# Performance work log

Hardware: AMD Instinct MI355X
Metric: run time of the kernel (lower is better)

Reference implementation:

```python
import jax, jax.numpy as jnp
import numpy as np
from jax import lax

J2 = -1.0
J4 = 0.5
KT = 0.5
DT = 0.01
SIGMA = float(np.sqrt(2.0 * KT * DT))  # noise scale per Euler-Maruyama step


def setup_inputs() -> dict:
    key = jax.random.key(0)
    k_x, = jax.random.split(key, 1)
    n_samples, n_dim = 2048, 256
    x0 = jax.random.normal(k_x, (n_samples, n_dim), dtype=jnp.float32)
    b = jnp.zeros((n_dim,), dtype=jnp.float32)  # learned bias parameter
    return {"x0": x0, "b": b, "n_steps": 500}


def reference(x0, b, n_steps):
    # Langevin dynamics: x <- x - grad_V(x)*dt + sqrt(2 kT dt)*N(0,1)
    # grad_V(x) = 2*J2*x + 4*J4*x^3 + b
    keys = jax.random.split(jax.random.key(1), n_steps)

    def step(x, k):
        grad = 2.0 * J2 * x + 4.0 * J4 * x * x * x + b
        noise = jax.random.normal(k, x.shape, x.dtype) * SIGMA
        return x - grad * DT + noise, None

    x, _ = lax.scan(step, x0, keys)
    return x
```

## Files before the change

### kernel.cpp

```cpp
#include <hip/hip_runtime.h>


__device__ __forceinline__ void tf2x32(unsigned k0, unsigned k1,
                                       unsigned c0, unsigned c1,
                                       unsigned& o0, unsigned& o1) {
  const unsigned k2 = k0 ^ k1 ^ 0x1BD11BDAu;
  unsigned x0 = c0 + k0, x1 = c1 + k1;
#define TF1(R) x0 += x1; x1 = ((x1 << (R)) | (x1 >> (32 - (R)))); x1 ^= x0;
  TF1(13) TF1(15) TF1(26) TF1(6)  x0 += k1; x1 += k2 + 1u;
  TF1(17) TF1(29) TF1(16) TF1(24) x0 += k2; x1 += k0 + 2u;
  TF1(13) TF1(15) TF1(26) TF1(6)  x0 += k0; x1 += k1 + 3u;
  TF1(17) TF1(29) TF1(16) TF1(24) x0 += k1; x1 += k2 + 4u;
  TF1(13) TF1(15) TF1(26) TF1(6)  x0 += k2; x1 += k0 + 5u;
#undef TF1
  o0 = x0; o1 = x1;
}

__device__ __forceinline__ void tf_fold2k(const unsigned wa[8],
                                          const unsigned wb[8], unsigned cj,
                                          unsigned& ra, unsigned& rb) {
  unsigned a0 = wa[0], a1 = cj + wa[1];
  unsigned b0 = wb[0], b1 = cj + wb[1];
#define TFR2(R)                                   \
  a0 += a1; b0 += b1;                             \
  a1 = ((a1 << (R)) | (a1 >> (32 - (R)))) ^ a0;   \
  b1 = ((b1 << (R)) | (b1 >> (32 - (R)))) ^ b0;
#define TFINJ2(i0, i1) a0 += wa[i0]; b0 += wb[i0]; a1 += wa[i1]; b1 += wb[i1];
  TFR2(13) TFR2(15) TFR2(26) TFR2(6)  TFINJ2(1, 3)
  TFR2(17) TFR2(29) TFR2(16) TFR2(24) TFINJ2(2, 4)
  TFR2(13) TFR2(15) TFR2(26) TFR2(6)  TFINJ2(0, 5)
  TFR2(17) TFR2(29) TFR2(16) TFR2(24) TFINJ2(1, 6)
  TFR2(13) TFR2(15) TFR2(26) TFR2(6)  TFINJ2(2, 7)
#undef TFR2
#undef TFINJ2
  ra = a0 ^ a1;
  rb = b0 ^ b1;
}

__device__ __forceinline__ void b2n2(unsigned bba, unsigned bbb,
                                     float& na, float& nb) {
  const float fa = __uint_as_float((bba >> 9) | 0x3F800000u) - 1.0f;
  const float fb = __uint_as_float((bbb >> 9) | 0x3F800000u) - 1.0f;
  const float ua = fmaf(fa, 2.0f, -0.99999994f);
  const float ub = fmaf(fb, 2.0f, -0.99999994f);
  const float ma = ua * ua, mb = ub * ub;
  const float la = __log2f(1.0f - ma);
  const float lb = __log2f(1.0f - mb);
  const float wa = la * -0.693147180559945f;
  const float wb = lb * -0.693147180559945f;
  const bool sa = wa < 5.0f, sb = wb < 5.0f;
  const float za = sa ? (wa - 2.5f) : (__builtin_amdgcn_sqrtf(wa) - 3.0f);
  const float zb = sb ? (wb - 2.5f) : (__builtin_amdgcn_sqrtf(wb) - 3.0f);
  float pa =           sa ? 2.81022636e-08f  : -0.000200214257f;
  float pb =           sb ? 2.81022636e-08f  : -0.000200214257f;
  pa = fmaf(pa, za,    sa ? 3.43273939e-07f  :  0.000100950558f);
  pb = fmaf(pb, zb,    sb ? 3.43273939e-07f  :  0.000100950558f);
  pa = fmaf(pa, za,    sa ? -3.5233877e-06f  :  0.00134934322f);
  pb = fmaf(pb, zb,    sb ? -3.5233877e-06f  :  0.00134934322f);
  pa = fmaf(pa, za,    sa ? -4.39150654e-06f : -0.00367342844f);
  pb = fmaf(pb, zb,    sb ? -4.39150654e-06f : -0.00367342844f);
  pa = fmaf(pa, za,    sa ? 0.00021858087f   :  0.00573950773f);
  pb = fmaf(pb, zb,    sb ? 0.00021858087f   :  0.00573950773f);
  pa = fmaf(pa, za,    sa ? -0.00125372503f  : -0.0076224613f);
  pb = fmaf(pb, zb,    sb ? -0.00125372503f  : -0.0076224613f);
  pa = fmaf(pa, za,    sa ? -0.00417768164f  :  0.00943887047f);
  pb = fmaf(pb, zb,    sb ? -0.00417768164f  :  0.00943887047f);
  pa = fmaf(pa, za,    sa ? 0.246640727f     :  1.00167406f);
  pb = fmaf(pb, zb,    sb ? 0.246640727f     :  1.00167406f);
  pa = fmaf(pa, za,    sa ? 1.50140941f      :  2.83297682f);
  pb = fmaf(pb, zb,    sb ? 1.50140941f      :  2.83297682f);
  na = __uint_as_float(0x3FB504F3u) * (pa * ua);
  nb = __uint_as_float(0x3FB504F3u) * (pb * ub);
}

__global__ __launch_bounds__(256, 8) void langevin_tf(
    const float* __restrict__ x0p, const float* __restrict__ bias,
    const int* __restrict__ nsteps_p, float* __restrict__ out,
    int N, int ndim) {
  __shared__ __align__(16) unsigned skeys[512 * 8];
  const int n_steps = __builtin_amdgcn_readfirstlane(nsteps_p[0]);
  const int nfill = n_steps < 512 ? n_steps : 512;
  for (int l = (int)threadIdx.x; l < nfill; l += (int)blockDim.x) {
    unsigned o0, o1;
    tf2x32(0u, 1u, 0u, (unsigned)l, o0, o1);
    const unsigned k2 = o0 ^ o1 ^ 0x1BD11BDAu;
    unsigned* wp = &skeys[8 * l];
    wp[0] = o0;       wp[1] = o1;       wp[2] = k2;       wp[3] = k2 + 1u;
    wp[4] = o0 + 2u;  wp[5] = o1 + 3u;  wp[6] = k2 + 4u;  wp[7] = o0 + 5u;
  }
  __syncthreads();

  const int j = (int)(blockIdx.x * blockDim.x + threadIdx.x);
  if (j >= N) return;
  const unsigned cj = (unsigned)j;
  float x = x0p[j];
  const float b = bias[j % ndim];

  if (n_steps <= 512) {
    const uint4* sk4 = (const uint4*)skeys;
    int t = 0;
#pragma unroll 1
    for (; t + 1 < n_steps; t += 2) {
      const uint4 a_lo = sk4[2 * t + 0], a_hi = sk4[2 * t + 1];
      const uint4 b_lo = sk4[2 * t + 2], b_hi = sk4[2 * t + 3];
      const unsigned wa[8] = {a_lo.x, a_lo.y, a_lo.z, a_lo.w,
                              a_hi.x, a_hi.y, a_hi.z, a_hi.w};
      const unsigned wb[8] = {b_lo.x, b_lo.y, b_lo.z, b_lo.w,
                              b_hi.x, b_hi.y, b_hi.z, b_hi.w};
      unsigned ra, rb;
      tf_fold2k(wa, wb, cj, ra, rb);
      float na, nb;
      b2n2(ra, rb, na, nb);
      float g = -2.0f * x + ((2.0f * x) * x) * x + b;
      x = (x - g * 0.01f) + na * 0.1f;
      g = -2.0f * x + ((2.0f * x) * x) * x + b;
      x = (x - g * 0.01f) + nb * 0.1f;
    }
    if (t < n_steps) {
      const uint4 a_lo = sk4[2 * t + 0], a_hi = sk4[2 * t + 1];
      const unsigned wa[8] = {a_lo.x, a_lo.y, a_lo.z, a_lo.w,
                              a_hi.x, a_hi.y, a_hi.z, a_hi.w};
      unsigned ra, rb;
      tf_fold2k(wa, wa, cj, ra, rb);
      float na, nb;
      b2n2(ra, ra, na, nb);
      const float g = -2.0f * x + ((2.0f * x) * x) * x + b;
      x = (x - g * 0.01f) + na * 0.1f;
    }
  } else {
    for (int t = 0; t < n_steps; t += 2) {
      unsigned oa0, oa1, ob0, ob1;
      tf2x32(0u, 1u, 0u, (unsigned)t, oa0, oa1);
      tf2x32(0u, 1u, 0u, (unsigned)(t + 1), ob0, ob1);
      const unsigned ka2 = oa0 ^ oa1 ^ 0x1BD11BDAu;
      const unsigned kb2 = ob0 ^ ob1 ^ 0x1BD11BDAu;
      const unsigned wa[8] = {oa0, oa1, ka2, ka2 + 1u, oa0 + 2u, oa1 + 3u,
                              ka2 + 4u, oa0 + 5u};
      const unsigned wb[8] = {ob0, ob1, kb2, kb2 + 1u, ob0 + 2u, ob1 + 3u,
                              kb2 + 4u, ob0 + 5u};
      unsigned ra, rb;
      tf_fold2k(wa, wb, cj, ra, rb);
      float na, nb;
      b2n2(ra, rb, na, nb);
      float g = -2.0f * x + ((2.0f * x) * x) * x + b;
      x = (x - g * 0.01f) + na * 0.1f;
      if (t + 1 < n_steps) {
        g = -2.0f * x + ((2.0f * x) * x) * x + b;
        x = (x - g * 0.01f) + nb * 0.1f;
      }
    }
  }
  out[j] = x;
}

extern "C" void kernel_launch(void* const* d_in, const int* in_sizes, int n_in,
                              void* d_out, int out_size, void* d_ws, size_t ws_size,
                              hipStream_t stream) {
  (void)n_in; (void)d_ws; (void)ws_size; (void)out_size;
  const float* x0 = (const float*)d_in[0];
  const float* b = (const float*)d_in[1];
  const int* ns = (const int*)d_in[2];
  float* out = (float*)d_out;

  const int n = in_sizes[0];
  const int ndim = in_sizes[1];
  const int block = 256;
  const int grid = (n + block - 1) / block;
  hipLaunchKernelGGL(langevin_tf, dim3(grid), dim3(block), 0, stream,
                     x0, b, ns, out, n, ndim);
}
```

Baseline: 593.1 us.

## Shrink per-step key table, pack normal transform into float2, use 128-thread blocks

The shared-memory key table now holds only the two raw key words per step, and the derived key schedule is recomputed inside the Threefry fold with a few extra ALU ops. This replaces two 16-byte LDS loads per step with one and cuts the table from 16 KB to 4 KB. The Box-Muller style inverse-erf polynomial is written with two-wide float vectors so the compiler can emit packed FMA instructions. Block size drops from 256 to 128 threads, doubling the number of blocks for the 2048 samples, at the cost of more redundant key-table fills per block.

```diff
diff --git a/kernel.cpp b/kernel.cpp
--- a/kernel.cpp
+++ b/kernel.cpp
@@ -1,5 +1,7 @@
 #include <hip/hip_runtime.h>
 
+
+typedef float v2f __attribute__((ext_vector_type(2)));
 
 __device__ __forceinline__ void tf2x32(unsigned k0, unsigned k1,
                                        unsigned c0, unsigned c1,
@@ -16,77 +18,78 @@
   o0 = x0; o1 = x1;
 }
 
-__device__ __forceinline__ void tf_fold2k(const unsigned wa[8],
-                                          const unsigned wb[8], unsigned cj,
+__device__ __forceinline__ void tf_fold2k(unsigned ka0, unsigned ka1,
+                                          unsigned kb0, unsigned kb1,
+                                          unsigned cj,
                                           unsigned& ra, unsigned& rb) {
-  unsigned a0 = wa[0], a1 = cj + wa[1];
-  unsigned b0 = wb[0], b1 = cj + wb[1];
+  const unsigned ka2 = ka0 ^ ka1 ^ 0x1BD11BDAu;
+  const unsigned kb2 = kb0 ^ kb1 ^ 0x1BD11BDAu;
+  unsigned a0 = ka0, a1 = cj + ka1;
+  unsigned b0 = kb0, b1 = cj + kb1;
 #define TFR2(R)                                   \
   a0 += a1; b0 += b1;                             \
   a1 = ((a1 << (R)) | (a1 >> (32 - (R)))) ^ a0;   \
   b1 = ((b1 << (R)) | (b1 >> (32 - (R)))) ^ b0;
-#define TFINJ2(i0, i1) a0 += wa[i0]; b0 += wb[i0]; a1 += wa[i1]; b1 += wb[i1];
-  TFR2(13) TFR2(15) TFR2(26) TFR2(6)  TFINJ2(1, 3)
-  TFR2(17) TFR2(29) TFR2(16) TFR2(24) TFINJ2(2, 4)
-  TFR2(13) TFR2(15) TFR2(26) TFR2(6)  TFINJ2(0, 5)
-  TFR2(17) TFR2(29) TFR2(16) TFR2(24) TFINJ2(1, 6)
-  TFR2(13) TFR2(15) TFR2(26) TFR2(6)  TFINJ2(2, 7)
+  TFR2(13) TFR2(15) TFR2(26) TFR2(6)
+  a0 += ka1; b0 += kb1; a1 += ka2 + 1u; b1 += kb2 + 1u;
+  TFR2(17) TFR2(29) TFR2(16) TFR2(24)
+  a0 += ka2; b0 += kb2; a1 += ka0 + 2u; b1 += kb0 + 2u;
+  TFR2(13) TFR2(15) TFR2(26) TFR2(6)
+  a0 += ka0; b0 += kb0; a1 += ka1 + 3u; b1 += kb1 + 3u;
+  TFR2(17) TFR2(29) TFR2(16) TFR2(24)
+  a0 += ka1; b0 += kb1; a1 += ka2 + 4u; b1 += kb2 + 4u;
+  TFR2(13) TFR2(15) TFR2(26) TFR2(6)
+  a0 += ka2; b0 += kb2; a1 += ka0 + 5u; b1 += kb0 + 5u;
 #undef TFR2
-#undef TFINJ2
   ra = a0 ^ a1;
   rb = b0 ^ b1;
 }
 
 __device__ __forceinline__ void b2n2(unsigned bba, unsigned bbb,
                                      float& na, float& nb) {
-  const float fa = __uint_as_float((bba >> 9) | 0x3F800000u) - 1.0f;
-  const float fb = __uint_as_float((bbb >> 9) | 0x3F800000u) - 1.0f;
-  const float ua = fmaf(fa, 2.0f, -0.99999994f);
-  const float ub = fmaf(fb, 2.0f, -0.99999994f);
-  const float ma = ua * ua, mb = ub * ub;
-  const float la = __log2f(1.0f - ma);
-  const float lb = __log2f(1.0f - mb);
-  const float wa = la * -0.693147180559945f;
-  const float wb = lb * -0.693147180559945f;
-  const bool sa = wa < 5.0f, sb = wb < 5.0f;
-  const float za = sa ? (wa - 2.5f) : (__builtin_amdgcn_sqrtf(wa) - 3.0f);
-  const float zb = sb ? (wb - 2.5f) : (__builtin_amdgcn_sqrtf(wb) - 3.0f);
-  float pa =           sa ? 2.81022636e-08f  : -0.000200214257f;
-  float pb =           sb ? 2.81022636e-08f  : -0.000200214257f;
-  pa = fmaf(pa, za,    sa ? 3.43273939e-07f  :  0.000100950558f);
-  pb = fmaf(pb, zb,    sb ? 3.43273939e-07f  :  0.000100950558f);
-  pa = fmaf(pa, za,    sa ? -3.5233877e-06f  :  0.00134934322f);
-  pb = fmaf(pb, zb,    sb ? -3.5233877e-06f  :  0.00134934322f);
-  pa = fmaf(pa, za,    sa ? -4.39150654e-06f : -0.00367342844f);
-  pb = fmaf(pb, zb,    sb ? -4.39150654e-06f : -0.00367342844f);
-  pa = fmaf(pa, za,    sa ? 0.00021858087f   :  0.00573950773f);
-  pb = fmaf(pb, zb,    sb ? 0.00021858087f   :  0.00573950773f);
-  pa = fmaf(pa, za,    sa ? -0.00125372503f  : -0.0076224613f);
-  pb = fmaf(pb, zb,    sb ? -0.00125372503f  : -0.0076224613f);
-  pa = fmaf(pa, za,    sa ? -0.00417768164f  :  0.00943887047f);
-  pb = fmaf(pb, zb,    sb ? -0.00417768164f  :  0.00943887047f);
-  pa = fmaf(pa, za,    sa ? 0.246640727f     :  1.00167406f);
-  pb = fmaf(pb, zb,    sb ? 0.246640727f     :  1.00167406f);
-  pa = fmaf(pa, za,    sa ? 1.50140941f      :  2.83297682f);
-  pb = fmaf(pb, zb,    sb ? 1.50140941f      :  2.83297682f);
-  na = __uint_as_float(0x3FB504F3u) * (pa * ua);
-  nb = __uint_as_float(0x3FB504F3u) * (pb * ub);
+  v2f f;
+  f.x = __uint_as_float((bba >> 9) | 0x3F800000u) - 1.0f;
+  f.y = __uint_as_float((bbb >> 9) | 0x3F800000u) - 1.0f;
+  const v2f u = __builtin_elementwise_fma(f, (v2f)2.0f, (v2f)(-0.99999994f));
+  const v2f m = u * u;
+  const v2f tt = (v2f)1.0f - m;
+  v2f l;
+  l.x = __log2f(tt.x);
+  l.y = __log2f(tt.y);
+  const v2f w = l * (v2f)(-0.693147180559945f);
+  const bool sa = w.x < 5.0f, sb = w.y < 5.0f;
+  const v2f zc = w - (v2f)2.5f;
+  v2f z;
+  z.x = sa ? zc.x : (__builtin_amdgcn_sqrtf(w.x) - 3.0f);
+  z.y = sb ? zc.y : (__builtin_amdgcn_sqrtf(w.y) - 3.0f);
+#define SEL2(A, B) (v2f){sa ? (A) : (B), sb ? (A) : (B)}
+  v2f p = SEL2(2.81022636e-08f, -0.000200214257f);
+  p = __builtin_elementwise_fma(p, z, SEL2(3.43273939e-07f, 0.000100950558f));
+  p = __builtin_elementwise_fma(p, z, SEL2(-3.5233877e-06f, 0.00134934322f));
+  p = __builtin_elementwise_fma(p, z, SEL2(-4.39150654e-06f, -0.00367342844f));
+  p = __builtin_elementwise_fma(p, z, SEL2(0.00021858087f, 0.00573950773f));
+  p = __builtin_elementwise_fma(p, z, SEL2(-0.00125372503f, -0.0076224613f));
+  p = __builtin_elementwise_fma(p, z, SEL2(-0.00417768164f, 0.00943887047f));
+  p = __builtin_elementwise_fma(p, z, SEL2(0.246640727f, 1.00167406f));
+  p = __builtin_elementwise_fma(p, z, SEL2(1.50140941f, 2.83297682f));
+#undef SEL2
+  const v2f n = (p * u) * (v2f)__uint_as_float(0x3FB504F3u);
+  na = n.x;
+  nb = n.y;
 }
 
-__global__ __launch_bounds__(256, 8) void langevin_tf(
+__global__ __launch_bounds__(128, 8) void langevin_tf(
     const float* __restrict__ x0p, const float* __restrict__ bias,
     const int* __restrict__ nsteps_p, float* __restrict__ out,
     int N, int ndim) {
-  __shared__ __align__(16) unsigned skeys[512 * 8];
+  __shared__ __align__(16) unsigned skeys[512 * 2];
   const int n_steps = __builtin_amdgcn_readfirstlane(nsteps_p[0]);
   const int nfill = n_steps < 512 ? n_steps : 512;
   for (int l = (int)threadIdx.x; l < nfill; l += (int)blockDim.x) {
     unsigned o0, o1;
     tf2x32(0u, 1u, 0u, (unsigned)l, o0, o1);
-    const unsigned k2 = o0 ^ o1 ^ 0x1BD11BDAu;
-    unsigned* wp = &skeys[8 * l];
-    wp[0] = o0;       wp[1] = o1;       wp[2] = k2;       wp[3] = k2 + 1u;
-    wp[4] = o0 + 2u;  wp[5] = o1 + 3u;  wp[6] = k2 + 4u;  wp[7] = o0 + 5u;
+    skeys[2 * l] = o0;
+    skeys[2 * l + 1] = o1;
   }
   __syncthreads();
 
@@ -101,14 +104,9 @@
     int t = 0;
 #pragma unroll 1
     for (; t + 1 < n_steps; t += 2) {
-      const uint4 a_lo = sk4[2 * t + 0], a_hi = sk4[2 * t + 1];
-      const uint4 b_lo = sk4[2 * t + 2], b_hi = sk4[2 * t + 3];
-      const unsigned wa[8] = {a_lo.x, a_lo.y, a_lo.z, a_lo.w,
-                              a_hi.x, a_hi.y, a_hi.z, a_hi.w};
-      const unsigned wb[8] = {b_lo.x, b_lo.y, b_lo.z, b_lo.w,
-                              b_hi.x, b_hi.y, b_hi.z, b_hi.w};
+      const uint4 kk = sk4[t >> 1];
       unsigned ra, rb;
-      tf_fold2k(wa, wb, cj, ra, rb);
+      tf_fold2k(kk.x, kk.y, kk.z, kk.w, cj, ra, rb);
       float na, nb;
       b2n2(ra, rb, na, nb);
       float g = -2.0f * x + ((2.0f * x) * x) * x + b;
@@ -117,11 +115,9 @@
       x = (x - g * 0.01f) + nb * 0.1f;
     }
     if (t < n_steps) {
-      const uint4 a_lo = sk4[2 * t + 0], a_hi = sk4[2 * t + 1];
-      const unsigned wa[8] = {a_lo.x, a_lo.y, a_lo.z, a_lo.w,
-                              a_hi.x, a_hi.y, a_hi.z, a_hi.w};
+      const unsigned o0 = skeys[2 * t], o1 = skeys[2 * t + 1];
       unsigned ra, rb;
-      tf_fold2k(wa, wa, cj, ra, rb);
+      tf_fold2k(o0, o1, o0, o1, cj, ra, rb);
       float na, nb;
       b2n2(ra, ra, na, nb);
       const float g = -2.0f * x + ((2.0f * x) * x) * x + b;
@@ -132,14 +128,8 @@
       unsigned oa0, oa1, ob0, ob1;
       tf2x32(0u, 1u, 0u, (unsigned)t, oa0, oa1);
       tf2x32(0u, 1u, 0u, (unsigned)(t + 1), ob0, ob1);
-      const unsigned ka2 = oa0 ^ oa1 ^ 0x1BD11BDAu;
-      const unsigned kb2 = ob0 ^ ob1 ^ 0x1BD11BDAu;
-      const unsigned wa[8] = {oa0, oa1, ka2, ka2 + 1u, oa0 + 2u, oa1 + 3u,
-                              ka2 + 4u, oa0 + 5u};
-      const unsigned wb[8] = {ob0, ob1, kb2, kb2 + 1u, ob0 + 2u, ob1 + 3u,
-                              kb2 + 4u, ob0 + 5u};
       unsigned ra, rb;
-      tf_fold2k(wa, wb, cj, ra, rb);
+      tf_fold2k(oa0, oa1, ob0, ob1, cj, ra, rb);
       float na, nb;
       b2n2(ra, rb, na, nb);
       float g = -2.0f * x + ((2.0f * x) * x) * x + b;
@@ -164,7 +154,7 @@
 
   const int n = in_sizes[0];
   const int ndim = in_sizes[1];
-  const int block = 256;
+  const int block = 128;
   const int grid = (n + block - 1) / block;
   hipLaunchKernelGGL(langevin_tf, dim3(grid), dim3(block), 0, stream,
                      x0, b, ns, out, n, ndim);
```

After: 681.6 us. 14.9% more time.
